# Kernel optimization log

Measured on AMD Instinct MI355X. Metric: run time of the kernel, lower is better.

Reference implementation:

```python
import jax, jax.numpy as jnp
import numpy as np

D_IN = 1024
D_OUT = 1024

def setup_inputs() -> dict:
    key = jax.random.key(0)
    kx, kq, kk, kv = jax.random.split(key, 4)
    X = jax.random.normal(kx, (4, 2048, D_IN), dtype=jnp.float32)
    s = 1.0 / np.sqrt(D_IN)
    Wq = jax.random.uniform(kq, (D_IN, D_OUT), jnp.float32, -s, s)
    Wk = jax.random.uniform(kk, (D_IN, D_OUT), jnp.float32, -s, s)
    Wv = jax.random.uniform(kv, (D_IN, D_OUT), jnp.float32, -s, s)
    return {"X": X, "Wq": Wq, "Wk": Wk, "Wv": Wv}

def reference(X, Wq, Wk, Wv):
    # X: [b, s, d_in]; W*: [d_in, d_out] (torch Linear weight transposed)
    B, S, _ = X.shape
    q = jnp.einsum('bsd,de->bse', X, Wq)
    k = jnp.einsum('bsd,de->bse', X, Wk)
    v = jnp.einsum('bsd,de->bse', X, Wv)
    scores = jnp.einsum('bqe,bke->bqk', q, k)  # [b, s, s]
    causal = jnp.triu(jnp.ones((S, S), dtype=bool), k=1)
    scores = jnp.where(causal, -jnp.inf, scores)
    weights = jax.nn.softmax(scores / jnp.sqrt(jnp.asarray(k.shape[-1], scores.dtype)), axis=-1)
    # dropout p=0.0 (eval) -> identity
    return jnp.einsum('bqk,bke->bqe', weights, v)
```

## Files before the change

kernel.cpp:

```cpp
#include <hip/hip_runtime.h>
#include <cstdint>
#include <cmath>

typedef unsigned short u16;
typedef u16   u16x4  __attribute__((ext_vector_type(4)));
typedef u16   u16x8  __attribute__((ext_vector_type(8)));
typedef __bf16 bf16x8 __attribute__((ext_vector_type(8)));
typedef float f32x4  __attribute__((ext_vector_type(4)));

__device__ __forceinline__ u16 f2bf(float f) {
    uint32_t u = __builtin_bit_cast(uint32_t, f);
    u += 0x7fffu + ((u >> 16) & 1u);
    return (u16)(u >> 16);
}
__device__ __forceinline__ float bf2f(u16 v) {
    uint32_t u = ((uint32_t)v) << 16;
    return __builtin_bit_cast(float, u);
}
__device__ __forceinline__ void gload_lds16(const u16* g, u16* l) {
    __builtin_amdgcn_global_load_lds((const __attribute__((address_space(1))) void*)g,
                                     (__attribute__((address_space(3))) void*)l,
                                     16, 0, 0);
}

__global__ __launch_bounds__(256) void prep_kernel(const float* __restrict__ X,
                                                   const float* __restrict__ Wq,
                                                   const float* __restrict__ Wk,
                                                   const float* __restrict__ Wv,
                                                   u16* __restrict__ Xb,
                                                   u16* __restrict__ Wt) {
    __shared__ u16 tile[64 * 72];
    typedef float f4 __attribute__((ext_vector_type(4)));
    const int bid = blockIdx.x;
    if (bid < 8192) {
        const int idx = bid * 256 + threadIdx.x;
        f4 f = ((const f4*)X)[idx];
        u16x4 o;
        o[0] = f2bf(f[0]); o[1] = f2bf(f[1]); o[2] = f2bf(f[2]); o[3] = f2bf(f[3]);
        ((u16x4*)Xb)[idx] = o;
        return;
    }
    const int id = bid - 8192;
    const int z = id >> 8, rem = id & 255;
    const float* W = (z == 0) ? Wq : (z == 1) ? Wk : Wv;
    u16* out = Wt + ((size_t)z << 20);
    const int nt = (rem & 15) * 64, kt = (rem >> 4) * 64;
    const int t = threadIdx.x, r = t >> 2, cq = (t & 3) * 16;
    const float* src = W + (size_t)(kt + r) * 1024 + nt + cq;
#pragma unroll
    for (int q = 0; q < 4; q++) {
        f4 f = ((const f4*)src)[q];
        tile[r * 72 + cq + q * 4 + 0] = f2bf(f[0]);
        tile[r * 72 + cq + q * 4 + 1] = f2bf(f[1]);
        tile[r * 72 + cq + q * 4 + 2] = f2bf(f[2]);
        tile[r * 72 + cq + q * 4 + 3] = f2bf(f[3]);
    }
    __syncthreads();
    u16x8 o0, o1;
#pragma unroll
    for (int e = 0; e < 8; e++) { o0[e] = tile[(cq + e) * 72 + r]; o1[e] = tile[(cq + 8 + e) * 72 + r]; }
    u16* dst = out + (size_t)(nt + r) * 1024 + kt + cq;
    *(u16x8*)dst = o0;
    *(u16x8*)(dst + 8) = o1;
}

template <int OUTMODE>
__device__ __forceinline__ void gemm_bt_core(u16* __restrict__ smem,
                                             const u16* __restrict__ A,
                                             const u16* __restrict__ Bt,
                                             void* __restrict__ outp,
                                             const int ldk, const int ldo,
                                             const int kbeg, const int kend,
                                             const int m0, const int n0,
                                             const int om0, const int on0) {
    u16* As = smem;
    u16* Bs = smem + 4096;
    const int tid = (int)threadIdx.x;
    const int wave = tid >> 6, lane = tid & 63;
    const int wm = wave >> 1, wn = wave & 1;

    f32x4 acc[4][4] = {};

    const int sr = lane >> 2;
    const int scw = ((lane & 3) ^ ((sr >> 1) & 3)) * 8;
    const u16* gA = A  + (size_t)(m0 + wave * 32 + sr) * ldk + scw;
    const u16* gB = Bt + (size_t)(n0 + wave * 32 + sr) * ldk + scw;
    u16* lA = As + wave * 1024;
    u16* lB = Bs + wave * 1024;
    const size_t rstep = (size_t)ldk * 16;

    const int arow = lane & 15;
    const int ksw  = (arow >> 1) & 3;
    const int koff = (((lane >> 4) ^ ksw)) * 8;
    const u16* pa = As + (wm * 64 + arow) * 32 + koff;
    const u16* pb = Bs + (wn * 64 + arow) * 32 + koff;

    for (int k0 = kbeg; k0 < kend; k0 += 32) {
        gload_lds16(gA + k0,         lA);
        gload_lds16(gA + k0 + rstep, lA + 512);
        gload_lds16(gB + k0,         lB);
        gload_lds16(gB + k0 + rstep, lB + 512);
        __syncthreads();
        bf16x8 a[4], b[4];
#pragma unroll
        for (int i = 0; i < 4; i++) a[i] = *(const bf16x8*)(pa + i * 512);
#pragma unroll
        for (int j = 0; j < 4; j++) b[j] = *(const bf16x8*)(pb + j * 512);
#pragma unroll
        for (int i = 0; i < 4; i++)
#pragma unroll
            for (int j = 0; j < 4; j++)
                acc[i][j] = __builtin_amdgcn_mfma_f32_16x16x32_bf16(a[i], b[j], acc[i][j], 0, 0, 0);
        __syncthreads();
    }

    const int row0 = om0 + wm * 64 + ((lane >> 4) << 2);
    const int col0 = on0 + wn * 64 + (lane & 15);
    if constexpr (OUTMODE == 0) {
        u16* o = (u16*)outp;
#pragma unroll
        for (int i = 0; i < 4; i++)
#pragma unroll
            for (int r = 0; r < 4; r++) {
                u16* po = o + (size_t)(row0 + i * 16 + r) * ldo + col0;
#pragma unroll
                for (int j = 0; j < 4; j++) po[j * 16] = f2bf(acc[i][j][r]);
            }
    } else {
        float* o = (float*)outp;
#pragma unroll
        for (int i = 0; i < 4; i++)
#pragma unroll
            for (int r = 0; r < 4; r++) {
                float* po = o + (size_t)(row0 + i * 16 + r) * ldo + col0;
#pragma unroll
                for (int j = 0; j < 4; j++) po[j * 16] = acc[i][j][r];
            }
    }
}

__global__ __launch_bounds__(512, 2) void qkv_gemm_kernel(const u16* __restrict__ Xb,
                                                          const u16* __restrict__ Wt,
                                                          u16* __restrict__ QKV) {
    __shared__ u16 lds[65536];
    const int bid = blockIdx.x;
    const int xcd = bid & 7, slot = bid >> 3;
    const int m0 = (xcd * 8 + (slot >> 3)) << 7;
    const int n0 = (slot & 7) << 7;

    const int tid = (int)threadIdx.x;
    const int w = tid >> 6, l = tid & 63;
    const int wm = w >> 2, wn = w & 3;

    const int srow = w * 16 + (l >> 3);
    const int scol = ((l & 7) ^ ((l >> 3) & 7)) * 8;
    const u16* gA  = Xb + (size_t)(m0 + srow) * 1024 + scol;
    const u16* gB0 = Wt + (size_t)(n0 + srow) * 1024 + scol;
    const u16* gB1 = gB0 + ((size_t)1 << 20);
    const u16* gB2 = gB0 + ((size_t)2 << 20);
    u16* const sA = lds + w * 1024;
    u16* const sB = lds + 16384 + w * 1024;

    const int c0 = ((l >> 4) ^ (l & 7)) * 8;
    const u16* const pa_ = lds + (wm * 64 + (l & 15)) * 64;
    const u16* const pb_ = lds + 16384 + (wn * 32 + (l & 15)) * 64;

    f32x4 acc[3][4][2] = {};
    bf16x8 a[4][2], b[2][2];

#define MFMA_ __builtin_amdgcn_mfma_f32_16x16x32_bf16
#define STG_A(P, T) \
    gload_lds16(gA + (size_t)(T) * 64,                    sA + (P) * 8192); \
    gload_lds16(gA + (size_t)(T) * 64 + (size_t)8 * 1024, sA + (P) * 8192 + 512);
#define STG_B(P, Z, GB, T) \
    gload_lds16(GB + (size_t)(T) * 64,                    sB + (Z) * 16384 + (P) * 8192); \
    gload_lds16(GB + (size_t)(T) * 64 + (size_t)8 * 1024, sB + (Z) * 16384 + (P) * 8192 + 512);
#define LD_A(P) \
    _Pragma("unroll") for (int m_ = 0; m_ < 4; m_++) { \
        a[m_][0] = *(const bf16x8*)(pa_ + (P) * 8192 + m_ * 1024 + c0); \
        a[m_][1] = *(const bf16x8*)(pa_ + (P) * 8192 + m_ * 1024 + (c0 ^ 32)); \
    }
#define LD_B(P, Z) \
    _Pragma("unroll") for (int n_ = 0; n_ < 2; n_++) { \
        b[n_][0] = *(const bf16x8*)(pb_ + (Z) * 16384 + (P) * 8192 + n_ * 1024 + c0); \
        b[n_][1] = *(const bf16x8*)(pb_ + (Z) * 16384 + (P) * 8192 + n_ * 1024 + (c0 ^ 32)); \
    }
#define MM(Z) \
    _Pragma("unroll") for (int m_ = 0; m_ < 4; m_++) { \
        _Pragma("unroll") for (int n_ = 0; n_ < 2; n_++) { \
            acc[Z][m_][n_] = MFMA_(a[m_][0], b[n_][0], acc[Z][m_][n_], 0, 0, 0); \
            acc[Z][m_][n_] = MFMA_(a[m_][1], b[n_][1], acc[Z][m_][n_], 0, 0, 0); \
        } \
    }
#define VM6 asm volatile("s_waitcnt vmcnt(6)" ::: "memory");
#define VM0 asm volatile("s_waitcnt vmcnt(0)" ::: "memory");
#define VMN
#define BAR __builtin_amdgcn_s_barrier();
#define PRIO1 __builtin_amdgcn_s_setprio(1);
#define PRIO0 __builtin_amdgcn_s_setprio(0);
#define TILE(P, S1, T1, S2, T2, VM3) \
    LD_A(P) LD_B(P, 0) \
    if (S1) { STG_B((P) ^ 1, 2, gB2, T1) } \
    BAR PRIO1 MM(0) PRIO0 BAR \
    LD_B(P, 1) \
    if (S2) { STG_A(P, T2) STG_B(P, 0, gB0, T2) } \
    BAR PRIO1 MM(1) PRIO0 BAR \
    LD_B(P, 2) \
    if (S2) { STG_B(P, 1, gB1, T2) } \
    VM3 \
    BAR PRIO1 MM(2) PRIO0 BAR

    STG_A(0, 0) STG_B(0, 0, gB0, 0) STG_B(0, 1, gB1, 0) STG_B(0, 2, gB2, 0)
    STG_A(1, 1) STG_B(1, 0, gB0, 1) STG_B(1, 1, gB1, 1)
    asm volatile("s_waitcnt vmcnt(6)" ::: "memory");
    __builtin_amdgcn_s_barrier();

#pragma unroll 1
    for (int i = 0; i < 7; ++i) {
        TILE(0, 1, 2 * i + 1, 1, 2 * i + 2, VM6)
        TILE(1, 1, 2 * i + 2, 1, 2 * i + 3, VM6)
    }
    TILE(0, 1, 15, 0, 0, VM0)
    TILE(1, 0, 0, 0, 0, VMN)

    const int row0 = m0 + wm * 64 + ((l >> 4) << 2);
    const int col0 = n0 + wn * 32 + (l & 15);
#pragma unroll
    for (int z = 0; z < 3; z++) {
        u16* C = QKV + ((size_t)z << 23);
#pragma unroll
        for (int m = 0; m < 4; m++)
#pragma unroll
            for (int r = 0; r < 4; r++) {
                u16* po = C + (size_t)(row0 + m * 16 + r) * 1024 + col0;
#pragma unroll
                for (int n = 0; n < 2; n++) po[n * 16] = f2bf(acc[z][m][n][r]);
            }
    }
#undef MFMA_
#undef STG_A
#undef STG_B
#undef LD_A
#undef LD_B
#undef MM
#undef VM6
#undef VM0
#undef VMN
#undef BAR
#undef PRIO1
#undef PRIO0
#undef TILE
}

__global__ __launch_bounds__(256) void s_tr_kernel(const u16* __restrict__ QKV,
                                                   u16* __restrict__ S,
                                                   u16* __restrict__ Vt) {
    __shared__ u16 smem[8192];
    const int bid = blockIdx.x;
    if (bid < 576) {
        const int xcd = bid & 7, slot = bid >> 3;
        const int b = xcd >> 1, half = xcd & 1;
        int it = half ? 11 : 0;
        const int ntiles = half ? 70 : 66;
        if (slot >= ntiles) return;
        int acc = 0;
        while (acc + it + 1 <= slot) { acc += it + 1; it++; }
        const int jt = slot - acc;
        const u16* Q  = QKV + ((size_t)b << 21);
        const u16* Kp = QKV + ((size_t)1 << 23) + ((size_t)b << 21);
        gemm_bt_core<0>(smem, Q, Kp, S + ((size_t)b << 22), 1024, 2048, 0, 1024,
                        it * 128, jt * 128, it * 128, jt * 128);
        return;
    }
    const int id = bid - 576;
    const int z = id >> 9, rem = id & 511;
    const u16* src = QKV + ((size_t)2 << 23) + ((size_t)z << 21);
    u16* dst = Vt + ((size_t)z << 21);
    const int st = (rem & 31) * 64, et = (rem >> 5) * 64;
    u16 (*tile)[72] = (u16(*)[72])smem;
    const int t = threadIdx.x, r = t >> 2, cq = (t & 3) * 16;
    const u16* p = src + (size_t)(st + r) * 1024 + et + cq;
    u16x8 u0 = *(const u16x8*)p;
    u16x8 u1 = *(const u16x8*)(p + 8);
#pragma unroll
    for (int e = 0; e < 8; e++) { tile[r][cq + e] = u0[e]; tile[r][cq + 8 + e] = u1[e]; }
    __syncthreads();
    u16x8 o0, o1;
#pragma unroll
    for (int e = 0; e < 8; e++) { o0[e] = tile[cq + e][r]; o1[e] = tile[cq + 8 + e][r]; }
    u16* q = dst + (size_t)(et + r) * 2048 + st + cq;
    *(u16x8*)q = o0;
    *(u16x8*)(q + 8) = o1;
}

__device__ __forceinline__ void pv_tile128(const u16* __restrict__ Pb,
                                           const u16* __restrict__ Vb,
                                           float* __restrict__ Ob,
                                           u16* __restrict__ lds,
                                           const int it, const int n0) {
    const int tid = (int)threadIdx.x;
    const int w = tid >> 6, l = tid & 63;
    const int wm = w >> 2, wn = w & 3;
    const int nk = 2 * (it + 1);
    const int m0 = it * 128;

    const int srow = w * 16 + (l >> 3);
    const int scol = ((l & 7) ^ ((l >> 3) & 7)) * 8;
    const u16* gA = Pb + (size_t)(m0 + srow) * 2048 + scol;
    const u16* gB = Vb + (size_t)(n0 + srow) * 2048 + scol;
    u16* const sA = lds + w * 1024;
    u16* const sB = lds + 24576 + w * 1024;

    const int c0 = ((l >> 4) ^ (l & 7)) * 8;
    const u16* const pa_ = lds + (wm * 64 + (l & 15)) * 64;
    const u16* const pb_ = lds + 24576 + (wn * 32 + (l & 15)) * 64;

    f32x4 acc[4][2] = {};

#define PSTG(T, BUF) \
    gload_lds16(gA + (size_t)(T) * 64,                    sA + (BUF) * 8192); \
    gload_lds16(gA + (size_t)(T) * 64 + (size_t)8 * 2048, sA + (BUF) * 8192 + 512); \
    gload_lds16(gB + (size_t)(T) * 64,                    sB + (BUF) * 8192); \
    gload_lds16(gB + (size_t)(T) * 64 + (size_t)8 * 2048, sB + (BUF) * 8192 + 512);

    PSTG(0, 0) PSTG(1, 1)
    asm volatile("s_waitcnt vmcnt(4)" ::: "memory");
    __builtin_amdgcn_s_barrier();

    int bufR = 0, bufW = 2;
#pragma unroll 1
    for (int t = 0; t < nk; ++t) {
        bf16x8 a[4][2], b[2][2];
#pragma unroll
        for (int m = 0; m < 4; m++) {
            a[m][0] = *(const bf16x8*)(pa_ + bufR * 8192 + m * 1024 + c0);
            a[m][1] = *(const bf16x8*)(pa_ + bufR * 8192 + m * 1024 + (c0 ^ 32));
        }
#pragma unroll
        for (int n = 0; n < 2; n++) {
            b[n][0] = *(const bf16x8*)(pb_ + bufR * 8192 + n * 1024 + c0);
            b[n][1] = *(const bf16x8*)(pb_ + bufR * 8192 + n * 1024 + (c0 ^ 32));
        }
        if (t < nk - 2) {
            PSTG(t + 2, bufW)
            asm volatile("s_waitcnt vmcnt(4)" ::: "memory");
        } else {
            asm volatile("s_waitcnt vmcnt(0)" ::: "memory");
        }
        __builtin_amdgcn_s_barrier();
        __builtin_amdgcn_s_setprio(1);
#pragma unroll
        for (int m = 0; m < 4; m++)
#pragma unroll
            for (int n = 0; n < 2; n++) {
                acc[m][n] = __builtin_amdgcn_mfma_f32_16x16x32_bf16(a[m][0], b[n][0], acc[m][n], 0, 0, 0);
                acc[m][n] = __builtin_amdgcn_mfma_f32_16x16x32_bf16(a[m][1], b[n][1], acc[m][n], 0, 0, 0);
            }
        __builtin_amdgcn_s_setprio(0);
        __builtin_amdgcn_s_barrier();
        bufR = (bufR == 2) ? 0 : bufR + 1;
        bufW = (bufW == 2) ? 0 : bufW + 1;
    }
#undef PSTG

    const int row0 = m0 + wm * 64 + ((l >> 4) << 2);
    const int col0 = n0 + wn * 32 + (l & 15);
#pragma unroll
    for (int m = 0; m < 4; m++)
#pragma unroll
        for (int r = 0; r < 4; r++) {
            float* po = Ob + (size_t)(row0 + m * 16 + r) * 1024 + col0;
#pragma unroll
            for (int n = 0; n < 2; n++) po[n * 16] = acc[m][n][r];
        }
}

__global__ __launch_bounds__(512, 2) void pv_gemm_kernel(const u16* __restrict__ P,
                                                         const u16* __restrict__ Vt,
                                                         float* __restrict__ O) {
    __shared__ u16 lds[49152];
    const int bid = blockIdx.x;
    const int xcd = bid & 7, slot = bid >> 3;
    const int combo = xcd * 4 + (slot >> 3);
    const int n0 = (slot & 7) * 128;
    const int pair = combo >> 2, b = combo & 3;
    const u16* Pb = P + ((size_t)b << 22);
    const u16* Vb = Vt + ((size_t)b << 21);
    float* Ob = O + ((size_t)b << 21);
    pv_tile128(Pb, Vb, Ob, lds, 15 - pair, n0);
    pv_tile128(Pb, Vb, Ob, lds, pair, n0);
}

__global__ __launch_bounds__(256) void softmax_kernel(u16* __restrict__ S) {
    const int wave = threadIdx.x >> 6, lane = threadIdx.x & 63;
    const int g = blockIdx.x * 4 + wave;
    const int b = g >> 11, i = g & 2047;
    u16* row = S + ((size_t)b << 22) + ((size_t)i << 11);
    const int n = i + 1;
    const int kend = ((i >> 7) + 1) << 7;
    const int nt_ = (kend + 511) >> 9;
    const float NEG = -1e30f;
    float v[32];
    float m = NEG;
#pragma unroll
    for (int t = 0; t < 4; t++) {
        if (t < nt_) {
            u16x8 u = *(const u16x8*)(row + t * 512 + lane * 8);
#pragma unroll
            for (int e = 0; e < 8; e++) {
                const int col = t * 512 + lane * 8 + e;
                float f = (col < n) ? bf2f(u[e]) : NEG;
                v[t * 8 + e] = f;
                m = fmaxf(m, f);
            }
        }
    }
#pragma unroll
    for (int off = 32; off > 0; off >>= 1) m = fmaxf(m, __shfl_xor(m, off, 64));
    const float sc = 0.03125f * 1.44269504088896f;
    float s = 0.f;
#pragma unroll
    for (int t = 0; t < 4; t++) {
        if (t < nt_) {
#pragma unroll
            for (int e = 0; e < 8; e++) {
                const float x = v[t * 8 + e];
                const float e2 = (x == NEG) ? 0.f : exp2f((x - m) * sc);
                v[t * 8 + e] = e2;
                s += e2;
            }
        }
    }
#pragma unroll
    for (int off = 32; off > 0; off >>= 1) s += __shfl_xor(s, off, 64);
    const float inv = 1.f / s;
#pragma unroll
    for (int t = 0; t < 4; t++) {
        if (t < nt_) {
            u16x8 o;
#pragma unroll
            for (int e = 0; e < 8; e++) o[e] = f2bf(v[t * 8 + e] * inv);
            *(u16x8*)(row + t * 512 + lane * 8) = o;
        }
    }
}

extern "C" void kernel_launch(void* const* d_in, const int* in_sizes, int n_in,
                              void* d_out, int out_size, void* d_ws, size_t ws_size,
                              hipStream_t stream) {
    const float* X  = (const float*)d_in[0];
    const float* Wq = (const float*)d_in[1];
    const float* Wk = (const float*)d_in[2];
    const float* Wv = (const float*)d_in[3];
    float* out = (float*)d_out;

    u16* ws  = (u16*)d_ws;
    u16* Xb  = ws;
    u16* Wt  = Xb + ((size_t)1 << 23);
    u16* QKV = Wt + 3 * ((size_t)1 << 20);
    u16* S   = QKV + 3 * ((size_t)1 << 23);
    u16* Vt  = Xb;

    prep_kernel<<<8960, 256, 0, stream>>>(X, Wq, Wk, Wv, Xb, Wt);
    qkv_gemm_kernel<<<512, 512, 0, stream>>>(Xb, Wt, QKV);
    s_tr_kernel<<<2624, 256, 0, stream>>>(QKV, S, Vt);
    softmax_kernel<<<2048, 256, 0, stream>>>(S);
    pv_gemm_kernel<<<256, 512, 0, stream>>>(S, Vt, out);
}
```

Before: 222.5 us.

## Fuse V transpose into QKV GEMM epilogue and rewrite QK^T GEMM kernel

The V transpose moves into the QKV projection epilogue, which stages V through LDS and writes it already transposed, so the separate transpose pass over V disappears. The QK^T score GEMM becomes its own kernel with 512 threads, 64-wide double-buffered K tiles, async global-to-LDS loads and MFMA priority hints, replacing the older 256-thread single-buffered core. This removes a kernel's worth of V reads and writes and should raise MFMA efficiency on the causal score tiles. The cost is extra LDS work and barriers in the QKV epilogue, plus a simpler block mapping for the score kernel that no longer places tiles per XCD.

```diff
diff --git a/kernel.cpp b/kernel.cpp
--- a/kernel.cpp
+++ b/kernel.cpp
@@ -64,84 +64,10 @@
     *(u16x8*)(dst + 8) = o1;
 }
 
-template <int OUTMODE>
-__device__ __forceinline__ void gemm_bt_core(u16* __restrict__ smem,
-                                             const u16* __restrict__ A,
-                                             const u16* __restrict__ Bt,
-                                             void* __restrict__ outp,
-                                             const int ldk, const int ldo,
-                                             const int kbeg, const int kend,
-                                             const int m0, const int n0,
-                                             const int om0, const int on0) {
-    u16* As = smem;
-    u16* Bs = smem + 4096;
-    const int tid = (int)threadIdx.x;
-    const int wave = tid >> 6, lane = tid & 63;
-    const int wm = wave >> 1, wn = wave & 1;
-
-    f32x4 acc[4][4] = {};
-
-    const int sr = lane >> 2;
-    const int scw = ((lane & 3) ^ ((sr >> 1) & 3)) * 8;
-    const u16* gA = A  + (size_t)(m0 + wave * 32 + sr) * ldk + scw;
-    const u16* gB = Bt + (size_t)(n0 + wave * 32 + sr) * ldk + scw;
-    u16* lA = As + wave * 1024;
-    u16* lB = Bs + wave * 1024;
-    const size_t rstep = (size_t)ldk * 16;
-
-    const int arow = lane & 15;
-    const int ksw  = (arow >> 1) & 3;
-    const int koff = (((lane >> 4) ^ ksw)) * 8;
-    const u16* pa = As + (wm * 64 + arow) * 32 + koff;
-    const u16* pb = Bs + (wn * 64 + arow) * 32 + koff;
-
-    for (int k0 = kbeg; k0 < kend; k0 += 32) {
-        gload_lds16(gA + k0,         lA);
-        gload_lds16(gA + k0 + rstep, lA + 512);
-        gload_lds16(gB + k0,         lB);
-        gload_lds16(gB + k0 + rstep, lB + 512);
-        __syncthreads();
-        bf16x8 a[4], b[4];
-#pragma unroll
-        for (int i = 0; i < 4; i++) a[i] = *(const bf16x8*)(pa + i * 512);
-#pragma unroll
-        for (int j = 0; j < 4; j++) b[j] = *(const bf16x8*)(pb + j * 512);
-#pragma unroll
-        for (int i = 0; i < 4; i++)
-#pragma unroll
-            for (int j = 0; j < 4; j++)
-                acc[i][j] = __builtin_amdgcn_mfma_f32_16x16x32_bf16(a[i], b[j], acc[i][j], 0, 0, 0);
-        __syncthreads();
-    }
-
-    const int row0 = om0 + wm * 64 + ((lane >> 4) << 2);
-    const int col0 = on0 + wn * 64 + (lane & 15);
-    if constexpr (OUTMODE == 0) {
-        u16* o = (u16*)outp;
-#pragma unroll
-        for (int i = 0; i < 4; i++)
-#pragma unroll
-            for (int r = 0; r < 4; r++) {
-                u16* po = o + (size_t)(row0 + i * 16 + r) * ldo + col0;
-#pragma unroll
-                for (int j = 0; j < 4; j++) po[j * 16] = f2bf(acc[i][j][r]);
-            }
-    } else {
-        float* o = (float*)outp;
-#pragma unroll
-        for (int i = 0; i < 4; i++)
-#pragma unroll
-            for (int r = 0; r < 4; r++) {
-                float* po = o + (size_t)(row0 + i * 16 + r) * ldo + col0;
-#pragma unroll
-                for (int j = 0; j < 4; j++) po[j * 16] = acc[i][j][r];
-            }
-    }
-}
-
 __global__ __launch_bounds__(512, 2) void qkv_gemm_kernel(const u16* __restrict__ Xb,
                                                           const u16* __restrict__ Wt,
-                                                          u16* __restrict__ QKV) {
+                                                          u16* __restrict__ QKV,
+                                                          u16* __restrict__ Vt) {
     __shared__ u16 lds[65536];
     const int bid = blockIdx.x;
     const int xcd = bid & 7, slot = bid >> 3;
@@ -226,7 +152,7 @@
     const int row0 = m0 + wm * 64 + ((l >> 4) << 2);
     const int col0 = n0 + wn * 32 + (l & 15);
 #pragma unroll
-    for (int z = 0; z < 3; z++) {
+    for (int z = 0; z < 2; z++) {
         u16* C = QKV + ((size_t)z << 23);
 #pragma unroll
         for (int m = 0; m < 4; m++)
@@ -234,8 +160,28 @@
             for (int r = 0; r < 4; r++) {
                 u16* po = C + (size_t)(row0 + m * 16 + r) * 1024 + col0;
 #pragma unroll
-                for (int n = 0; n < 2; n++) po[n * 16] = f2bf(acc[z][m][n][r]);
+                for (int n = 0; n < 2; n++) po[n * 16] = f2bf(acc[2 * 0 + z][m][n][r]);
             }
+    }
+    __syncthreads();
+    {
+        u16 (*tr)[136] = (u16(*)[136])lds;
+        const int rl = wm * 64 + ((l >> 4) << 2);
+        const int cl = wn * 32 + (l & 15);
+#pragma unroll
+        for (int m = 0; m < 4; m++)
+#pragma unroll
+            for (int r = 0; r < 4; r++)
+#pragma unroll
+                for (int n = 0; n < 2; n++)
+                    tr[cl + n * 16][rl + m * 16 + r] = f2bf(acc[2][m][n][r]);
+        __syncthreads();
+        const int e = tid >> 2, cc = (tid & 3) * 32;
+        const int b = m0 >> 11;
+        u16* dst = Vt + ((size_t)b << 21) + (size_t)(n0 + e) * 2048 + (m0 & 2047) + cc;
+#pragma unroll
+        for (int q = 0; q < 4; q++)
+            *(u16x8*)(dst + q * 8) = *(const u16x8*)(&tr[e][cc + q * 8]);
     }
 #undef MFMA_
 #undef STG_A
@@ -252,45 +198,83 @@
 #undef TILE
 }
 
-__global__ __launch_bounds__(256) void s_tr_kernel(const u16* __restrict__ QKV,
-                                                   u16* __restrict__ S,
-                                                   u16* __restrict__ Vt) {
-    __shared__ u16 smem[8192];
+__global__ __launch_bounds__(512, 2) void qk_gemm_kernel(const u16* __restrict__ QKV,
+                                                         u16* __restrict__ S) {
+    __shared__ u16 lds[32768];
     const int bid = blockIdx.x;
-    if (bid < 576) {
-        const int xcd = bid & 7, slot = bid >> 3;
-        const int b = xcd >> 1, half = xcd & 1;
-        int it = half ? 11 : 0;
-        const int ntiles = half ? 70 : 66;
-        if (slot >= ntiles) return;
-        int acc = 0;
-        while (acc + it + 1 <= slot) { acc += it + 1; it++; }
-        const int jt = slot - acc;
-        const u16* Q  = QKV + ((size_t)b << 21);
-        const u16* Kp = QKV + ((size_t)1 << 23) + ((size_t)b << 21);
-        gemm_bt_core<0>(smem, Q, Kp, S + ((size_t)b << 22), 1024, 2048, 0, 1024,
-                        it * 128, jt * 128, it * 128, jt * 128);
-        return;
-    }
-    const int id = bid - 576;
-    const int z = id >> 9, rem = id & 511;
-    const u16* src = QKV + ((size_t)2 << 23) + ((size_t)z << 21);
-    u16* dst = Vt + ((size_t)z << 21);
-    const int st = (rem & 31) * 64, et = (rem >> 5) * 64;
-    u16 (*tile)[72] = (u16(*)[72])smem;
-    const int t = threadIdx.x, r = t >> 2, cq = (t & 3) * 16;
-    const u16* p = src + (size_t)(st + r) * 1024 + et + cq;
-    u16x8 u0 = *(const u16x8*)p;
-    u16x8 u1 = *(const u16x8*)(p + 8);
-#pragma unroll
-    for (int e = 0; e < 8; e++) { tile[r][cq + e] = u0[e]; tile[r][cq + 8 + e] = u1[e]; }
-    __syncthreads();
-    u16x8 o0, o1;
-#pragma unroll
-    for (int e = 0; e < 8; e++) { o0[e] = tile[cq + e][r]; o1[e] = tile[cq + 8 + e][r]; }
-    u16* q = dst + (size_t)(et + r) * 2048 + st + cq;
-    *(u16x8*)q = o0;
-    *(u16x8*)(q + 8) = o1;
+    const int b = bid & 3;
+    int t = bid >> 2;
+    int it = 0;
+    { int acc_ = 0; while (acc_ + it + 1 <= t) { acc_ += it + 1; it++; } t -= acc_; }
+    const int jt = t;
+    const int m0 = it * 128, n0 = jt * 128;
+    const u16* Q = QKV + ((size_t)b << 21);
+    const u16* K = QKV + ((size_t)1 << 23) + ((size_t)b << 21);
+    u16* Sb = S + ((size_t)b << 22);
+
+    const int tid = (int)threadIdx.x, w = tid >> 6, l = tid & 63;
+    const int wm = w >> 2, wn = w & 3;
+    const int srow = w * 16 + (l >> 3);
+    const int scol = ((l & 7) ^ ((l >> 3) & 7)) * 8;
+    const u16* gA = Q + (size_t)(m0 + srow) * 1024 + scol;
+    const u16* gB = K + (size_t)(n0 + srow) * 1024 + scol;
+    u16* const sA = lds + w * 1024;
+    u16* const sB = lds + 16384 + w * 1024;
+    const int c0 = ((l >> 4) ^ (l & 7)) * 8;
+    const u16* const pa_ = lds + (wm * 64 + (l & 15)) * 64;
+    const u16* const pb_ = lds + 16384 + (wn * 32 + (l & 15)) * 64;
+
+    f32x4 acc[4][2] = {};
+#define QSTG(T, BUF) \
+    gload_lds16(gA + (size_t)(T) * 64,                    sA + (BUF) * 8192); \
+    gload_lds16(gA + (size_t)(T) * 64 + (size_t)8 * 1024, sA + (BUF) * 8192 + 512); \
+    gload_lds16(gB + (size_t)(T) * 64,                    sB + (BUF) * 8192); \
+    gload_lds16(gB + (size_t)(T) * 64 + (size_t)8 * 1024, sB + (BUF) * 8192 + 512);
+
+    QSTG(0, 0)
+#pragma unroll 1
+    for (int kt = 0; kt < 16; ++kt) {
+        if (kt < 15) {
+            QSTG(kt + 1, (kt + 1) & 1)
+            asm volatile("s_waitcnt vmcnt(4)" ::: "memory");
+        } else {
+            asm volatile("s_waitcnt vmcnt(0)" ::: "memory");
+        }
+        __builtin_amdgcn_s_barrier();
+        const int rb = (kt & 1) * 8192;
+        bf16x8 a[4][2], bb[2][2];
+#pragma unroll
+        for (int m = 0; m < 4; m++) {
+            a[m][0] = *(const bf16x8*)(pa_ + rb + m * 1024 + c0);
+            a[m][1] = *(const bf16x8*)(pa_ + rb + m * 1024 + (c0 ^ 32));
+        }
+#pragma unroll
+        for (int n = 0; n < 2; n++) {
+            bb[n][0] = *(const bf16x8*)(pb_ + rb + n * 1024 + c0);
+            bb[n][1] = *(const bf16x8*)(pb_ + rb + n * 1024 + (c0 ^ 32));
+        }
+        __builtin_amdgcn_s_setprio(1);
+#pragma unroll
+        for (int m = 0; m < 4; m++)
+#pragma unroll
+            for (int n = 0; n < 2; n++) {
+                acc[m][n] = __builtin_amdgcn_mfma_f32_16x16x32_bf16(a[m][0], bb[n][0], acc[m][n], 0, 0, 0);
+                acc[m][n] = __builtin_amdgcn_mfma_f32_16x16x32_bf16(a[m][1], bb[n][1], acc[m][n], 0, 0, 0);
+            }
+        __builtin_amdgcn_s_setprio(0);
+        __builtin_amdgcn_s_barrier();
+    }
+#undef QSTG
+    const int row0 = m0 + wm * 64 + ((l >> 4) << 2);
+    const int col0 = n0 + wn * 32 + (l & 15);
+#pragma unroll
+    for (int m = 0; m < 4; m++)
+#pragma unroll
+        for (int r = 0; r < 4; r++) {
+            u16* po = Sb + (size_t)(row0 + m * 16 + r) * 2048 + col0;
+#pragma unroll
+            for (int n = 0; n < 2; n++) po[n * 16] = f2bf(acc[m][n][r]);
+        }
 }
 
 __device__ __forceinline__ void pv_tile128(const u16* __restrict__ Pb,
@@ -459,11 +443,11 @@
     u16* Wt  = Xb + ((size_t)1 << 23);
     u16* QKV = Wt + 3 * ((size_t)1 << 20);
     u16* S   = QKV + 3 * ((size_t)1 << 23);
-    u16* Vt  = Xb;
+    u16* Vt  = QKV + ((size_t)2 << 23);
 
     prep_kernel<<<8960, 256, 0, stream>>>(X, Wq, Wk, Wv, Xb, Wt);
-    qkv_gemm_kernel<<<512, 512, 0, stream>>>(Xb, Wt, QKV);
-    s_tr_kernel<<<2624, 256, 0, stream>>>(QKV, S, Vt);
+    qkv_gemm_kernel<<<512, 512, 0, stream>>>(Xb, Wt, QKV, Vt);
+    qk_gemm_kernel<<<544, 512, 0, stream>>>(QKV, S);
     softmax_kernel<<<2048, 256, 0, stream>>>(S);
     pv_gemm_kernel<<<256, 512, 0, stream>>>(S, Vt, out);
 }
```

Measured after the change: 224.9 us. About the same (+1.1%).
